# Kernel optimization log

Hardware: AMD Instinct MI355X
Metric: run time of the kernel (lower is better)

The kernel has to match this reference:

```python
import jax, jax.numpy as jnp
import numpy as np

S, N, D = 65536, 8192, 128  # images, texts, embed dim


def setup_inputs() -> dict:
    key = jax.random.key(0)
    k1, k2, k3 = jax.random.split(key, 3)
    return {
        "image_features": jax.random.normal(k1, (S, D), dtype=jnp.float32),
        "text_features": jax.random.normal(k2, (N, D), dtype=jnp.float32),
        "key": jax.random.randint(k3, (S,), 0, N),
        "logit_scale": jnp.asarray(10.0, dtype=jnp.float32),  # already exponentiated temperature
        "logit_bias": jnp.asarray(-10.0, dtype=jnp.float32),
    }


def _l2norm(x):
    return x / (jnp.linalg.norm(x, ord=2, axis=-1, keepdims=True) + 1e-12)


def reference(image_features, text_features, key, logit_scale, logit_bias):
    s = image_features.shape[0]
    n = text_features.shape[0]
    zimg = _l2norm(image_features)           # (s, d)
    ztxt = _l2norm(text_features)            # (n, d)

    # True-positive logits: only the diagonal gather of the full (s, n) matmul is used,
    # so compute it directly as a row-wise dot product.
    tp_logits = jnp.einsum("sd,sd->s", zimg, ztxt[key]) * logit_scale + logit_bias
    pot_losses = jax.nn.softplus(-tp_logits)  # (s,)

    # Segmented argmin over images grouped by their text key (pick_best_candidate=True).
    seg_min = jax.ops.segment_min(pot_losses, key, num_segments=n)        # (n,)
    counts = jax.ops.segment_sum(jnp.ones((s,), jnp.int32), key, num_segments=n)
    valid = counts > 0                                                    # (n,)
    is_min = pot_losses == seg_min[key]
    cand_idx = jnp.where(is_min, jnp.arange(s), s)                        # first-occurrence tie-break
    best = jax.ops.segment_min(cand_idx, key, num_segments=n)             # (n,)
    best = jnp.where(valid, best, 0)

    zimg_sel = jnp.where(valid[:, None], zimg[best], 0.0)                 # (n, d)

    logits = zimg_sel @ ztxt.T * logit_scale + logit_bias                 # (n, n)
    diag = jnp.eye(n, dtype=bool)
    # labels*logits == logits on diagonal, -logits off-diagonal; softplus(-labels*logits):
    terms = jax.nn.softplus(jnp.where(diag, -logits, logits))
    mask = valid[:, None] & valid[None, :]
    num_valid = jnp.sum(valid)
    loss = jnp.sum(jnp.where(mask, terms, 0.0)) / jnp.maximum(num_valid, 1).astype(terms.dtype)
    return loss
```

## Files before the change

### kernel.cpp

```cpp
#include <hip/hip_runtime.h>
#include <stdint.h>

#define D 128

typedef __attribute__((ext_vector_type(4))) float float4v;
typedef long long frag8;

__device__ __forceinline__ float hw_exp2(float x) { return __builtin_amdgcn_exp2f(x); }
__device__ __forceinline__ float hw_log2(float x) { return __builtin_amdgcn_logf(x); }

__device__ __forceinline__ float softplus_fast(float x) {
    float e = hw_exp2(x * 1.44269504f);
    return 0.69314718f * hw_log2(1.0f + e);
}

__device__ __forceinline__ unsigned short f2fp8x2(float x, float y) {
    int p = __builtin_amdgcn_cvt_pk_fp8_f32(x, y, 0, false);
    return (unsigned short)(p & 0xFFFF);
}

__device__ __forceinline__ float dot4(float4 a, float4 b) {
    return a.x * b.x + a.y * b.y + a.z * b.z + a.w * b.w;
}

__device__ __forceinline__ void gload_lds16(const uint8_t* g, uint8_t* l) {
    __builtin_amdgcn_global_load_lds(
        (const __attribute__((address_space(1))) void*)g,
        (__attribute__((address_space(3))) void*)l, 16, 0, 0);
}

__device__ __forceinline__ int swz_col(int c, int row) {
    return c ^ ((row & 15) << 3);
}

__global__ __launch_bounds__(256) void k_prep(const float* __restrict__ img,
                                              const float* __restrict__ txt,
                                              const int* __restrict__ key,
                                              const float* __restrict__ sc,
                                              const float* __restrict__ bi,
                                              uint8_t* __restrict__ ztxt_f8,
                                              unsigned long long* __restrict__ packed,
                                              int nPack, int S) {
    const int t = threadIdx.x;
    if ((int)blockIdx.x < nPack) {
        int wave = t >> 6, lane = t & 63;
        int n = blockIdx.x * 4 + wave;
        const float2 v = *(const float2*)(txt + (size_t)n * D + lane * 2);
        float ss = v.x * v.x + v.y * v.y;
        #pragma unroll
        for (int off = 32; off; off >>= 1) ss += __shfl_xor(ss, off);
        float inv = 1.0f / (sqrtf(ss) + 1e-12f);
        *(unsigned short*)(ztxt_f8 + (size_t)n * D + swz_col(lane * 2, n)) =
            f2fp8x2(v.x * inv, v.y * inv);
    } else {
        int grp = t >> 4, gl = t & 15;
        int s = ((int)blockIdx.x - nPack) * 16 + grp;
        if (s < S) {
            int k = key[s];
            const float4* ia = (const float4*)(img + (size_t)s * D);
            const float4* tb = (const float4*)(txt + (size_t)k * D);
            float4 a0 = ia[gl], a1 = ia[16 + gl];
            float4 b0 = tb[gl], b1 = tb[16 + gl];
            float ss = dot4(a0, a0) + dot4(a1, a1);
            float dt = dot4(a0, b0) + dot4(a1, b1);
            float tt = dot4(b0, b0) + dot4(b1, b1);
            #pragma unroll
            for (int off = 8; off; off >>= 1) {
                ss += __shfl_xor(ss, off);
                dt += __shfl_xor(dt, off);
                tt += __shfl_xor(tt, off);
            }
            if (gl == 0) {
                float inv_i = 1.0f / (sqrtf(ss) + 1e-12f);
                float inv_t = 1.0f / (sqrtf(tt) + 1e-12f);
                float tp = dt * inv_i * inv_t * (*sc) + (*bi);
                float pot = softplus_fast(-tp);
                unsigned long long p =
                    ((unsigned long long)__float_as_uint(pot) << 32) | (unsigned int)s;
                atomicMin(&packed[k], p);
            }
        }
    }
}

__global__ __launch_bounds__(256) void k_select(const float* __restrict__ img,
                                               const unsigned long long* __restrict__ packed,
                                               uint8_t* __restrict__ zsel_f8,
                                               float* __restrict__ validF,
                                               double* __restrict__ partial,
                                               unsigned int* __restrict__ counter) {
    int t = threadIdx.x;
    if (blockIdx.x == 0) {
        partial[t] = 0.0;
        if (t == 0) *counter = 0u;
    }
    int wave = t >> 6;
    int lane = t & 63;
    int n = blockIdx.x * 4 + wave;
    unsigned long long p = packed[n];
    bool valid = (p != ~0ull);
    if (!valid) {
        if (lane == 0) validF[n] = 0.0f;
        *(unsigned short*)(zsel_f8 + (size_t)n * D + swz_col(lane * 2, n)) = 0;
        return;
    }
    int s = (int)(unsigned int)(p & 0xFFFFFFFFull);
    const float2 a = *(const float2*)(img + (size_t)s * D + lane * 2);
    float ss = a.x * a.x + a.y * a.y;
    #pragma unroll
    for (int off = 32; off; off >>= 1) ss += __shfl_xor(ss, off);
    float inv = 1.0f / (sqrtf(ss) + 1e-12f);
    *(unsigned short*)(zsel_f8 + (size_t)n * D + swz_col(lane * 2, n)) =
        f2fp8x2(a.x * inv, a.y * inv);
    if (lane == 0) validF[n] = 1.0f;
}

__global__ __launch_bounds__(512, 4) void k_gemm(const uint8_t* __restrict__ A,
                                                 const uint8_t* __restrict__ B,
                                                 const float* __restrict__ validF,
                                                 const float* __restrict__ sc,
                                                 const float* __restrict__ bi,
                                                 double* __restrict__ partial,
                                                 unsigned int* __restrict__ counter,
                                                 float* __restrict__ out, int N) {
    __shared__ __align__(16) uint8_t As[256 * 128];
    __shared__ __align__(16) uint8_t Bs[128 * 128];
    __shared__ float vI[256];
    __shared__ float vJ[128];
    __shared__ float wsum[8];
    __shared__ float fred[8];
    __shared__ double dred[8];
    __shared__ int lastB;

    const int t = threadIdx.x;
    const int i0 = blockIdx.y * 256;
    const int j0 = blockIdx.x * 128;

    if (t < 256) vI[t] = validF[i0 + t];
    else if (t < 384) vJ[t - 256] = validF[j0 + t - 256];

    const int wave = t >> 6, lane = t & 63;
    const int wm = (wave >> 1) * 64;
    const int wn = (wave & 1) * 64;
    const int lr = lane & 15;
    const int kq = (lane >> 4) * 8;
    const int swz = lr << 3;

    {
        const uint8_t* gA = A + (size_t)i0 * D;
        const uint8_t* gB = B + (size_t)j0 * D;
        #pragma unroll
        for (int j = 0; j < 4; ++j) {
            int L = wave * 4096 + j * 1024;
            gload_lds16(gA + L + lane * 16, As + L);
        }
        #pragma unroll
        for (int j = 0; j < 2; ++j) {
            int L = wave * 2048 + j * 1024;
            gload_lds16(gB + L + lane * 16, Bs + L);
        }
    }
    __syncthreads();

    float4v acc[4][4];
    #pragma unroll
    for (int mi = 0; mi < 4; ++mi)
        #pragma unroll
        for (int ni = 0; ni < 4; ++ni)
            acc[mi][ni] = (float4v){0.f, 0.f, 0.f, 0.f};

    #pragma unroll
    for (int k0 = 0; k0 < 128; k0 += 32) {
        const int col = (k0 + kq) ^ swz;
        frag8 bf[4];
        #pragma unroll
        for (int ni = 0; ni < 4; ++ni)
            bf[ni] = *(const frag8*)(Bs + (wn + ni * 16 + lr) * 128 + col);
        #pragma unroll
        for (int mi = 0; mi < 4; ++mi) {
            frag8 af = *(const frag8*)(As + (wm + mi * 16 + lr) * 128 + col);
            #pragma unroll
            for (int ni = 0; ni < 4; ++ni)
                acc[mi][ni] = __builtin_amdgcn_mfma_f32_16x16x32_fp8_fp8(
                    af, bf[ni], acc[mi][ni], 0, 0, 0);
        }
    }

    const float scale = *sc, bias = *bi;
    const float sl = scale * 1.44269504f, bl = bias * 1.44269504f;
    const int rb = (lane >> 4) * 4;
    float vjv[4], viv[4][4];
    #pragma unroll
    for (int ni = 0; ni < 4; ++ni) vjv[ni] = vJ[wn + ni * 16 + lr];
    #pragma unroll
    for (int mi = 0; mi < 4; ++mi)
        #pragma unroll
        for (int r = 0; r < 4; ++r) viv[mi][r] = vI[wm + mi * 16 + rb + r];

    float sum = 0.0f;
    if ((blockIdx.x >> 1) != blockIdx.y) {
        #pragma unroll
        for (int ni = 0; ni < 4; ++ni) {
            float s = 0.0f;
            #pragma unroll
            for (int mi = 0; mi < 4; ++mi)
                #pragma unroll
                for (int r = 0; r < 4; ++r) {
                    float u = hw_exp2(fmaf(acc[mi][ni][r], sl, bl));
                    s = fmaf(u, viv[mi][r], s);
                }
            sum = fmaf(s, vjv[ni], sum);
        }
    } else {
        const int dof = j0 - i0;
        #pragma unroll
        for (int ni = 0; ni < 4; ++ni) {
            float s = 0.0f;
            const int lj = wn + ni * 16 + lr;
            #pragma unroll
            for (int mi = 0; mi < 4; ++mi)
                #pragma unroll
                for (int r = 0; r < 4; ++r) {
                    const int li = wm + mi * 16 + rb + r;
                    float l = fmaf(acc[mi][ni][r], scale, bias);
                    float u = hw_exp2(-fabsf(l) * 1.44269504f);
                    float g = fmaxf(l, 0.0f) + fmaf(-0.5f * u, u, u);
                    if (li == lj + dof) g -= l;
                    s = fmaf(g, viv[mi][r], s);
                }
            sum = fmaf(s, vjv[ni], sum);
        }
    }
    #pragma unroll
    for (int off = 32; off; off >>= 1) sum += __shfl_xor(sum, off);
    if (lane == 0) wsum[wave] = sum;
    __syncthreads();
    if (t == 0) {
        float bs = 0.f;
        #pragma unroll
        for (int w = 0; w < 8; ++w) bs += wsum[w];
        atomicAdd(&partial[(blockIdx.y * gridDim.x + blockIdx.x) & 255], (double)bs);
        __threadfence();
        unsigned int v = atomicAdd(counter, 1u);
        lastB = (v == gridDim.x * gridDim.y - 1u);
    }
    __syncthreads();
    if (lastB) {
        float nv = 0.f;
        for (int i = t; i < N; i += 512) nv += validF[i];
        double ds = (t < 256) ? atomicAdd(&partial[t], 0.0) : 0.0;
        #pragma unroll
        for (int off = 32; off; off >>= 1) {
            nv += __shfl_xor(nv, off);
            ds += __shfl_xor(ds, off);
        }
        if (lane == 0) { fred[wave] = nv; dred[wave] = ds; }
        __syncthreads();
        if (t == 0) {
            float nvt = 0.f; double tot = 0.0;
            #pragma unroll
            for (int w = 0; w < 8; ++w) { nvt += fred[w]; tot += dred[w]; }
            if (nvt < 1.0f) nvt = 1.0f;
            out[0] = (float)(tot / (double)nvt);
        }
    }
}

extern "C" void kernel_launch(void* const* d_in, const int* in_sizes, int n_in,
                              void* d_out, int out_size, void* d_ws, size_t ws_size,
                              hipStream_t stream) {
    const float* img = (const float*)d_in[0];
    const float* txt = (const float*)d_in[1];
    const int*   key = (const int*)d_in[2];
    const float* sc  = (const float*)d_in[3];
    const float* bi  = (const float*)d_in[4];
    float* out = (float*)d_out;

    const int S = in_sizes[2];
    const int N = in_sizes[1] / D;

    char* ws = (char*)d_ws;
    size_t off = 0;
    auto carve = [&](size_t bytes) {
        void* p = ws + off;
        off = (off + bytes + 255) & ~(size_t)255;
        return p;
    };
    uint8_t*            ztxt_f8 = (uint8_t*)carve((size_t)N * D);
    uint8_t*            zsel_f8 = (uint8_t*)carve((size_t)N * D);
    unsigned long long* packed  = (unsigned long long*)carve((size_t)N * sizeof(unsigned long long));
    float*              validF  = (float*)carve((size_t)N * sizeof(float));
    double*             partial = (double*)carve(256 * sizeof(double));
    unsigned int*       counter = (unsigned int*)carve(sizeof(unsigned int));

    hipMemsetAsync(packed, 0xFF, (size_t)N * sizeof(unsigned long long), stream);

    const int nPack = N / 4;
    k_prep<<<nPack + (S + 15) / 16, 256, 0, stream>>>(img, txt, key, sc, bi,
                                                      ztxt_f8, packed, nPack, S);
    k_select<<<N / 4, 256, 0, stream>>>(img, packed, zsel_f8, validF, partial, counter);
    dim3 g(N / 128, N / 256);
    k_gemm<<<g, 512, 0, stream>>>(zsel_f8, ztxt_f8, validF, sc, bi, partial, counter, out, N);
}
```

Measured before the change: 138.6 us.

## Loop each GEMM block over four B tiles with double-buffered LDS, split final reduction

Each GEMM block now keeps its 256-row A tile resident and walks four consecutive 128-column B tiles. The next B tile is prefetched into a second LDS buffer while the current one is computed, which cuts the block count by four and reuses the A load across tiles. The last-block atomic counter reduction is replaced by a separate single-block finalize kernel. In exchange, per-block LDS rises (48KB) and there are fewer blocks to spread over the CUs, plus one extra kernel launch.

```diff
diff --git a/kernel.cpp b/kernel.cpp
--- a/kernel.cpp
+++ b/kernel.cpp
@@ -87,13 +87,9 @@
                                                const unsigned long long* __restrict__ packed,
                                                uint8_t* __restrict__ zsel_f8,
                                                float* __restrict__ validF,
-                                               double* __restrict__ partial,
-                                               unsigned int* __restrict__ counter) {
+                                               double* __restrict__ partial) {
     int t = threadIdx.x;
-    if (blockIdx.x == 0) {
-        partial[t] = 0.0;
-        if (t == 0) *counter = 0u;
-    }
+    if (blockIdx.x == 0) partial[t] = 0.0;
     int wave = t >> 6;
     int lane = t & 63;
     int n = blockIdx.x * 4 + wave;
@@ -120,24 +116,19 @@
                                                  const float* __restrict__ validF,
                                                  const float* __restrict__ sc,
                                                  const float* __restrict__ bi,
-                                                 double* __restrict__ partial,
-                                                 unsigned int* __restrict__ counter,
-                                                 float* __restrict__ out, int N) {
+                                                 double* __restrict__ partial) {
     __shared__ __align__(16) uint8_t As[256 * 128];
-    __shared__ __align__(16) uint8_t Bs[128 * 128];
+    __shared__ __align__(16) uint8_t Bs[2][128 * 128];
     __shared__ float vI[256];
-    __shared__ float vJ[128];
+    __shared__ float vJ[512];
     __shared__ float wsum[8];
-    __shared__ float fred[8];
-    __shared__ double dred[8];
-    __shared__ int lastB;
 
     const int t = threadIdx.x;
     const int i0 = blockIdx.y * 256;
-    const int j0 = blockIdx.x * 128;
-
+    const int j0 = blockIdx.x * 512;
+
+    vJ[t] = validF[j0 + t];
     if (t < 256) vI[t] = validF[i0 + t];
-    else if (t < 384) vJ[t - 256] = validF[j0 + t - 256];
 
     const int wave = t >> 6, lane = t & 63;
     const int wm = (wave >> 1) * 64;
@@ -146,9 +137,10 @@
     const int kq = (lane >> 4) * 8;
     const int swz = lr << 3;
 
+    const uint8_t* gA = A + (size_t)i0 * D;
+    const uint8_t* gB = B + (size_t)j0 * D;
+
     {
-        const uint8_t* gA = A + (size_t)i0 * D;
-        const uint8_t* gB = B + (size_t)j0 * D;
         #pragma unroll
         for (int j = 0; j < 4; ++j) {
             int L = wave * 4096 + j * 1024;
@@ -157,80 +149,99 @@
         #pragma unroll
         for (int j = 0; j < 2; ++j) {
             int L = wave * 2048 + j * 1024;
-            gload_lds16(gB + L + lane * 16, Bs + L);
+            gload_lds16(gB + L + lane * 16, Bs[0] + L);
         }
     }
     __syncthreads();
-
-    float4v acc[4][4];
-    #pragma unroll
-    for (int mi = 0; mi < 4; ++mi)
-        #pragma unroll
-        for (int ni = 0; ni < 4; ++ni)
-            acc[mi][ni] = (float4v){0.f, 0.f, 0.f, 0.f};
-
-    #pragma unroll
-    for (int k0 = 0; k0 < 128; k0 += 32) {
-        const int col = (k0 + kq) ^ swz;
-        frag8 bf[4];
-        #pragma unroll
-        for (int ni = 0; ni < 4; ++ni)
-            bf[ni] = *(const frag8*)(Bs + (wn + ni * 16 + lr) * 128 + col);
-        #pragma unroll
-        for (int mi = 0; mi < 4; ++mi) {
-            frag8 af = *(const frag8*)(As + (wm + mi * 16 + lr) * 128 + col);
-            #pragma unroll
-            for (int ni = 0; ni < 4; ++ni)
-                acc[mi][ni] = __builtin_amdgcn_mfma_f32_16x16x32_fp8_fp8(
-                    af, bf[ni], acc[mi][ni], 0, 0, 0);
-        }
-    }
 
     const float scale = *sc, bias = *bi;
     const float sl = scale * 1.44269504f, bl = bias * 1.44269504f;
     const int rb = (lane >> 4) * 4;
-    float vjv[4], viv[4][4];
-    #pragma unroll
-    for (int ni = 0; ni < 4; ++ni) vjv[ni] = vJ[wn + ni * 16 + lr];
+    float viv[4][4];
     #pragma unroll
     for (int mi = 0; mi < 4; ++mi)
         #pragma unroll
         for (int r = 0; r < 4; ++r) viv[mi][r] = vI[wm + mi * 16 + rb + r];
 
     float sum = 0.0f;
-    if ((blockIdx.x >> 1) != blockIdx.y) {
-        #pragma unroll
-        for (int ni = 0; ni < 4; ++ni) {
-            float s = 0.0f;
-            #pragma unroll
-            for (int mi = 0; mi < 4; ++mi)
+
+    #pragma unroll
+    for (int ji = 0; ji < 4; ++ji) {
+        if (ji < 3) {
+            const uint8_t* gS = gB + (ji + 1) * (128 * 128);
+            #pragma unroll
+            for (int j = 0; j < 2; ++j) {
+                int L = wave * 2048 + j * 1024;
+                gload_lds16(gS + L + lane * 16, Bs[(ji + 1) & 1] + L);
+            }
+        }
+        const uint8_t* Bc = Bs[ji & 1];
+
+        float4v acc[4][4];
+        #pragma unroll
+        for (int mi = 0; mi < 4; ++mi)
+            #pragma unroll
+            for (int ni = 0; ni < 4; ++ni)
+                acc[mi][ni] = (float4v){0.f, 0.f, 0.f, 0.f};
+
+        #pragma unroll
+        for (int k0 = 0; k0 < 128; k0 += 32) {
+            const int col = (k0 + kq) ^ swz;
+            frag8 bf[4];
+            #pragma unroll
+            for (int ni = 0; ni < 4; ++ni)
+                bf[ni] = *(const frag8*)(Bc + (wn + ni * 16 + lr) * 128 + col);
+            #pragma unroll
+            for (int mi = 0; mi < 4; ++mi) {
+                frag8 af = *(const frag8*)(As + (wm + mi * 16 + lr) * 128 + col);
                 #pragma unroll
-                for (int r = 0; r < 4; ++r) {
-                    float u = hw_exp2(fmaf(acc[mi][ni][r], sl, bl));
-                    s = fmaf(u, viv[mi][r], s);
-                }
-            sum = fmaf(s, vjv[ni], sum);
-        }
-    } else {
-        const int dof = j0 - i0;
-        #pragma unroll
-        for (int ni = 0; ni < 4; ++ni) {
-            float s = 0.0f;
-            const int lj = wn + ni * 16 + lr;
-            #pragma unroll
-            for (int mi = 0; mi < 4; ++mi)
+                for (int ni = 0; ni < 4; ++ni)
+                    acc[mi][ni] = __builtin_amdgcn_mfma_f32_16x16x32_fp8_fp8(
+                        af, bf[ni], acc[mi][ni], 0, 0, 0);
+            }
+        }
+
+        float vjv[4];
+        #pragma unroll
+        for (int ni = 0; ni < 4; ++ni) vjv[ni] = vJ[ji * 128 + wn + ni * 16 + lr];
+
+        const int jt = blockIdx.x * 4 + ji;
+        if ((jt >> 1) != blockIdx.y) {
+            #pragma unroll
+            for (int ni = 0; ni < 4; ++ni) {
+                float s = 0.0f;
                 #pragma unroll
-                for (int r = 0; r < 4; ++r) {
-                    const int li = wm + mi * 16 + rb + r;
-                    float l = fmaf(acc[mi][ni][r], scale, bias);
-                    float u = hw_exp2(-fabsf(l) * 1.44269504f);
-                    float g = fmaxf(l, 0.0f) + fmaf(-0.5f * u, u, u);
-                    if (li == lj + dof) g -= l;
-                    s = fmaf(g, viv[mi][r], s);
-                }
-            sum = fmaf(s, vjv[ni], sum);
-        }
-    }
+                for (int mi = 0; mi < 4; ++mi)
+                    #pragma unroll
+                    for (int r = 0; r < 4; ++r) {
+                        float u = hw_exp2(fmaf(acc[mi][ni][r], sl, bl));
+                        s = fmaf(u, viv[mi][r], s);
+                    }
+                sum = fmaf(s, vjv[ni], sum);
+            }
+        } else {
+            const int dof = (j0 + ji * 128) - i0;
+            #pragma unroll
+            for (int ni = 0; ni < 4; ++ni) {
+                float s = 0.0f;
+                const int lj = wn + ni * 16 + lr;
+                #pragma unroll
+                for (int mi = 0; mi < 4; ++mi)
+                    #pragma unroll
+                    for (int r = 0; r < 4; ++r) {
+                        const int li = wm + mi * 16 + rb + r;
+                        float l = fmaf(acc[mi][ni][r], scale, bias);
+                        float u = hw_exp2(-fabsf(l) * 1.44269504f);
+                        float g = fmaxf(l, 0.0f) + fmaf(-0.5f * u, u, u);
+                        if (li == lj + dof) g -= l;
+                        s = fmaf(g, viv[mi][r], s);
+                    }
+                sum = fmaf(s, vjv[ni], sum);
+            }
+        }
+        if (ji < 3) __syncthreads();
+    }
+
     #pragma unroll
     for (int off = 32; off; off >>= 1) sum += __shfl_xor(sum, off);
     if (lane == 0) wsum[wave] = sum;
@@ -240,29 +251,30 @@
         #pragma unroll
         for (int w = 0; w < 8; ++w) bs += wsum[w];
         atomicAdd(&partial[(blockIdx.y * gridDim.x + blockIdx.x) & 255], (double)bs);
-        __threadfence();
-        unsigned int v = atomicAdd(counter, 1u);
-        lastB = (v == gridDim.x * gridDim.y - 1u);
-    }
+    }
+}
+
+__global__ __launch_bounds__(256) void k_final(const double* __restrict__ partial,
+                                               const float* __restrict__ validF,
+                                               float* __restrict__ out, int N) {
+    __shared__ float wsum[4];
+    __shared__ double dsum[4];
+    int wave = threadIdx.x >> 6, lane = threadIdx.x & 63;
+    float s = 0.0f;
+    for (int i = threadIdx.x; i < N; i += 256) s += validF[i];
+    double d = partial[threadIdx.x];
+    #pragma unroll
+    for (int off = 32; off; off >>= 1) {
+        s += __shfl_xor(s, off);
+        d += __shfl_xor(d, off);
+    }
+    if (lane == 0) { wsum[wave] = s; dsum[wave] = d; }
     __syncthreads();
-    if (lastB) {
-        float nv = 0.f;
-        for (int i = t; i < N; i += 512) nv += validF[i];
-        double ds = (t < 256) ? atomicAdd(&partial[t], 0.0) : 0.0;
-        #pragma unroll
-        for (int off = 32; off; off >>= 1) {
-            nv += __shfl_xor(nv, off);
-            ds += __shfl_xor(ds, off);
-        }
-        if (lane == 0) { fred[wave] = nv; dred[wave] = ds; }
-        __syncthreads();
-        if (t == 0) {
-            float nvt = 0.f; double tot = 0.0;
-            #pragma unroll
-            for (int w = 0; w < 8; ++w) { nvt += fred[w]; tot += dred[w]; }
-            if (nvt < 1.0f) nvt = 1.0f;
-            out[0] = (float)(tot / (double)nvt);
-        }
+    if (threadIdx.x == 0) {
+        float nv = wsum[0] + wsum[1] + wsum[2] + wsum[3];
+        if (nv < 1.0f) nv = 1.0f;
+        double tot = dsum[0] + dsum[1] + dsum[2] + dsum[3];
+        out[0] = (float)(tot / (double)nv);
     }
 }
 
@@ -291,14 +303,14 @@
     unsigned long long* packed  = (unsigned long long*)carve((size_t)N * sizeof(unsigned long long));
     float*              validF  = (float*)carve((size_t)N * sizeof(float));
     double*             partial = (double*)carve(256 * sizeof(double));
-    unsigned int*       counter = (unsigned int*)carve(sizeof(unsigned int));
 
     hipMemsetAsync(packed, 0xFF, (size_t)N * sizeof(unsigned long long), stream);
 
     const int nPack = N / 4;
     k_prep<<<nPack + (S + 15) / 16, 256, 0, stream>>>(img, txt, key, sc, bi,
                                                       ztxt_f8, packed, nPack, S);
-    k_select<<<N / 4, 256, 0, stream>>>(img, packed, zsel_f8, validF, partial, counter);
-    dim3 g(N / 128, N / 256);
-    k_gemm<<<g, 512, 0, stream>>>(zsel_f8, ztxt_f8, validF, sc, bi, partial, counter, out, N);
-}
+    k_select<<<N / 4, 256, 0, stream>>>(img, packed, zsel_f8, validF, partial);
+    dim3 g(N / 512, N / 256);
+    k_gemm<<<g, 512, 0, stream>>>(zsel_f8, ztxt_f8, validF, sc, bi, partial);
+    k_final<<<1, 256, 0, stream>>>(partial, validF, out, N);
+}
```

After: 118.5 us. -14.5%, faster.
